# Kernel tuning notes

Hardware: AMD Instinct MI355X
Metric: run time of the kernel (lower is better)

The kernel has to match this reference:

```python
import jax, jax.numpy as jnp
import numpy as np

N = 32768      # nodes
E = 524288     # edges (avg degree 16)
F = 64         # node_feat_dim
D = 64         # gnn_dim (= per-head out channels, concat=False)
ED = 32        # edge_feat_dim
L = 6          # num_layers
H = 2          # heads
C = D          # per-head channels
LN_EPS = 1e-5


def layer_norm(h, g, b):
    mu = jnp.mean(h, axis=-1, keepdims=True)
    var = jnp.mean((h - mu) ** 2, axis=-1, keepdims=True)
    return g * (h - mu) * jax.lax.rsqrt(var + LN_EPS) + b


def setup_inputs() -> dict:
    key = jax.random.key(0)
    ks = jax.random.split(key, 16)
    x = jax.random.normal(ks[0], (N, F), jnp.float32)
    edge_index = jax.random.randint(ks[1], (2, E), 0, N, jnp.int32)
    edge_attr = jax.random.normal(ks[2], (E, ED), jnp.float32)
    manual_gamma = 1.0 + 0.1 * jax.random.normal(ks[3], (L, D), jnp.float32)
    manual_beta = 0.1 * jax.random.normal(ks[4], (L, D), jnp.float32)
    # node_embed Linear(F, D)
    embed_W = jax.random.normal(ks[5], (F, D), jnp.float32) / np.float32(np.sqrt(F))
    embed_b = jnp.zeros((D,), jnp.float32)
    # per-layer LayerNorm affine params
    ln_gamma = jnp.ones((L, D), jnp.float32)
    ln_beta = jnp.zeros((L, D), jnp.float32)
    # per-layer GATConv params (shared lin for src/dst, PyG non-bipartite)
    lin_W = jax.random.normal(ks[6], (L, D, H * C), jnp.float32) / np.float32(np.sqrt(D))
    lin_edge_W = jax.random.normal(ks[7], (L, ED, H * C), jnp.float32) / np.float32(np.sqrt(ED))
    att_src = jax.random.normal(ks[8], (L, H, C), jnp.float32) / np.float32(np.sqrt(C))
    att_dst = jax.random.normal(ks[9], (L, H, C), jnp.float32) / np.float32(np.sqrt(C))
    att_edge = jax.random.normal(ks[10], (L, H, C), jnp.float32) / np.float32(np.sqrt(C))
    gat_bias = jnp.zeros((L, C), jnp.float32)
    # edge output head: Linear(2D+ED, D) -> ReLU -> Linear(D, 1)
    head_W1 = jax.random.normal(ks[11], (2 * D + ED, D), jnp.float32) / np.float32(np.sqrt(2 * D + ED))
    head_b1 = jnp.zeros((D,), jnp.float32)
    head_W2 = jax.random.normal(ks[12], (D, 1), jnp.float32) / np.float32(np.sqrt(D))
    head_b2 = jnp.zeros((1,), jnp.float32)
    return dict(x=x, edge_index=edge_index, edge_attr=edge_attr,
                manual_gamma=manual_gamma, manual_beta=manual_beta,
                embed_W=embed_W, embed_b=embed_b, ln_gamma=ln_gamma, ln_beta=ln_beta,
                lin_W=lin_W, lin_edge_W=lin_edge_W, att_src=att_src, att_dst=att_dst,
                att_edge=att_edge, gat_bias=gat_bias, head_W1=head_W1, head_b1=head_b1,
                head_W2=head_W2, head_b2=head_b2)


def reference(x, edge_index, edge_attr, manual_gamma, manual_beta,
              embed_W, embed_b, ln_gamma, ln_beta, lin_W, lin_edge_W,
              att_src, att_dst, att_edge, gat_bias, head_W1, head_b1,
              head_W2, head_b2):
    src, dst = edge_index[0], edge_index[1]
    # PyG GATConv default add_self_loops=True, fill_value='mean' for edge_attr
    loop = jnp.arange(N, dtype=edge_index.dtype)
    src_f = jnp.concatenate([src, loop])   # [E+N]
    dst_f = jnp.concatenate([dst, loop])
    deg = jax.ops.segment_sum(jnp.ones((E,), x.dtype), dst, num_segments=N)
    loop_attr = jax.ops.segment_sum(edge_attr, dst, num_segments=N) / jnp.maximum(deg, 1.0)[:, None]
    edge_attr_f = jnp.concatenate([edge_attr, loop_attr], axis=0)  # [E+N, ED]

    h = x @ embed_W + embed_b  # [N, D]
    for l in range(L):
        hn = layer_norm(h, ln_gamma[l], ln_beta[l])
        hm = manual_gamma[l][None, :] * hn + manual_beta[l][None, :]
        xh = (hm @ lin_W[l]).reshape(N, H, C)                      # [N,H,C]
        a_s = jnp.sum(xh * att_src[l][None], axis=-1)              # [N,H]
        a_d = jnp.sum(xh * att_dst[l][None], axis=-1)              # [N,H]
        eh = (edge_attr_f @ lin_edge_W[l]).reshape(-1, H, C)       # [E+N,H,C]
        a_e = jnp.sum(eh * att_edge[l][None], axis=-1)             # [E+N,H]
        alpha = jax.nn.leaky_relu(a_s[src_f] + a_d[dst_f] + a_e, 0.2)
        amax = jax.ops.segment_max(alpha, dst_f, num_segments=N)   # every node has a self-loop
        ex = jnp.exp(alpha - amax[dst_f])
        den = jax.ops.segment_sum(ex, dst_f, num_segments=N)
        w = ex / (den[dst_f] + 1e-16)                              # segment softmax [E+N,H]
        msg = xh[src_f] * w[..., None]                             # [E+N,H,C]
        out = jax.ops.segment_sum(msg, dst_f, num_segments=N)      # [N,H,C]
        h = jax.nn.relu(jnp.mean(out, axis=1) + gat_bias[l])       # concat=False -> head mean

    ef = jnp.concatenate([h[src], h[dst], edge_attr], axis=-1)     # [E, 2D+ED]
    hid = jax.nn.relu(ef @ head_W1 + head_b1)
    return (hid @ head_W2 + head_b2)[:, 0]                         # [E]
```

## Files before the change

### kernel.cpp

```cpp
#include <hip/hip_runtime.h>
#include <hip/hip_bf16.h>
#include <math.h>

#define NN 32768
#define EE 524288
#define LL 6

typedef __attribute__((ext_vector_type(8))) short short8;
typedef __attribute__((ext_vector_type(4))) float floatx4;
typedef __attribute__((ext_vector_type(4))) float fx4;
typedef __attribute__((ext_vector_type(2))) float fx2;

union U16x8 { short8 v; unsigned short u[8]; };

__device__ __forceinline__ unsigned short f2bf(float x) {
    union { float f; unsigned int u; } v; v.f = x;
    unsigned int r = v.u + 0x7fffu + ((v.u >> 16) & 1u);
    return (unsigned short)(r >> 16);
}
__device__ __forceinline__ float bf2f(unsigned short h) {
    union { unsigned int u; float f; } v; v.u = (unsigned int)h << 16;
    return v.f;
}


__global__ void deg_kernel(const int* __restrict__ dst, int* __restrict__ deg) {
    int i = (blockIdx.x * 256 + threadIdx.x) * 4;
    int4 d = *(const int4*)(dst + i);
    atomicAdd(&deg[d.x], 1);
    atomicAdd(&deg[d.y], 1);
    atomicAdd(&deg[d.z], 1);
    atomicAdd(&deg[d.w], 1);
}

__global__ __launch_bounds__(1024) void scan_kernel(const int* __restrict__ deg,
                                                    int* __restrict__ row_ptr,
                                                    int* __restrict__ cnt) {
    __shared__ int bs[1024];
    int t = threadIdx.x;
    int base = t * 32;
    int loc[32];
    int s = 0;
#pragma unroll
    for (int i = 0; i < 32; ++i) { int v = deg[base + i]; loc[i] = s; s += v; }
    bs[t] = s;
    __syncthreads();
    for (int off = 1; off < 1024; off <<= 1) {
        int v = (t >= off) ? bs[t - off] : 0;
        __syncthreads();
        bs[t] += v;
        __syncthreads();
    }
    int pre = (t == 0) ? 0 : bs[t - 1];
#pragma unroll
    for (int i = 0; i < 32; ++i) { row_ptr[base + i] = pre + loc[i]; cnt[base + i] = 0; }
    if (t == 1023) row_ptr[NN] = bs[1023];
}

__global__ void fill_kernel(const int* __restrict__ src, const int* __restrict__ dst,
                            const int* __restrict__ row_ptr, int* __restrict__ cnt,
                            int2* __restrict__ sedge) {
    int e = blockIdx.x * 256 + threadIdx.x;
    if (e >= EE) return;
    int d = dst[e];
    int pos = row_ptr[d] + atomicAdd(&cnt[d], 1);
    sedge[pos] = make_int2(e, src[e]);
}

__global__ __launch_bounds__(256) void smallprep_kernel(
    const float* __restrict__ lin_W, const float* __restrict__ head_W1,
    const float* __restrict__ lin_edge_W, const float* __restrict__ att_edge,
    const float* __restrict__ att_src, const float* __restrict__ att_dst,
    unsigned short* __restrict__ gBhi, unsigned short* __restrict__ gBlo,
    unsigned short* __restrict__ aeBhi, unsigned short* __restrict__ aeBlo,
    float* __restrict__ vs, float* __restrict__ vvd,
    unsigned short* __restrict__ w1chi, unsigned short* __restrict__ w1clo,
    int* __restrict__ deg) {
    __shared__ float svb[384];
    int bb = blockIdx.x;
    int tid = threadIdx.x;
    if (bb < 7) {
        unsigned short* dh = gBhi + (size_t)bb * 128 * 64;
        unsigned short* dl = gBlo + (size_t)bb * 128 * 64;
        if (bb < 6) {
            int n2 = tid & 63, kh = tid >> 6;
            U16x8 hh[4], ll[4];
            for (int kk = 0; kk < 32; ++kk) {
                int j = kh * 32 + kk;
                int h = j >> 6, k = j & 63;
                float wv = 0.5f * lin_W[((size_t)bb * 64 + k) * 128 + h * 64 + n2];
                unsigned short h16 = f2bf(wv);
                hh[kk >> 3].u[kk & 7] = h16;
                ll[kk >> 3].u[kk & 7] = f2bf(wv - bf2f(h16));
            }
#pragma unroll
            for (int c = 0; c < 4; ++c) {
                int cg = kh * 4 + c;
                int off = n2 * 128 + ((cg ^ (n2 & 15)) << 3);
                *(short8*)(dh + off) = hh[c].v;
                *(short8*)(dl + off) = ll[c].v;
            }
        } else {
            int n = tid & 127, kh = tid >> 7;
            U16x8 hh[4], ll[4];
            for (int kk = 0; kk < 32; ++kk) {
                int k = kh * 32 + kk;
                float wv = (n < 64) ? head_W1[k * 64 + n] : head_W1[(64 + k) * 64 + (n - 64)];
                unsigned short h16 = f2bf(wv);
                hh[kk >> 3].u[kk & 7] = h16;
                ll[kk >> 3].u[kk & 7] = f2bf(wv - bf2f(h16));
            }
#pragma unroll
            for (int c = 0; c < 4; ++c) {
                int cg = kh * 4 + c;
                int off = n * 64 + ((cg ^ (n & 7)) << 3);
                *(short8*)(dh + off) = hh[c].v;
                *(short8*)(dl + off) = ll[c].v;
            }
        }
    } else if (bb == 7) {
        for (int t = tid; t < 384; t += 256) {
            int l = t / 64; int r = t & 63; int ed = r >> 1; int hh = r & 1;
            const float* w = lin_edge_W + l * 32 * 128 + ed * 128 + hh * 64;
            const float* a = att_edge + l * 128 + hh * 64;
            float s = 0.f;
#pragma unroll 8
            for (int c = 0; c < 64; ++c) s += w[c] * a[c];
            svb[t] = s;
        }
        int n = tid & 63, kc = tid >> 6;
#pragma unroll
        for (int j = 0; j < 8; ++j) {
            int k = kc * 8 + j;
            float wv = head_W1[(128 + k) * 64 + n];
            unsigned short h16 = f2bf(wv);
            w1chi[n * 32 + k] = h16;
            w1clo[n * 32 + k] = f2bf(wv - bf2f(h16));
        }
        __syncthreads();
        if (tid < 64) {
            int n2 = tid & 15, q = tid >> 4;
            U16x8 hi, lo;
#pragma unroll
            for (int i = 0; i < 8; ++i) {
                int k = q * 8 + i;
                float val = (n2 < 12) ? svb[(n2 >> 1) * 64 + k * 2 + (n2 & 1)] : 0.f;
                unsigned short h16 = f2bf(val);
                hi.u[i] = h16;
                lo.u[i] = f2bf(val - bf2f(h16));
            }
            *(short8*)(aeBhi + tid * 8) = hi.v;
            *(short8*)(aeBlo + tid * 8) = lo.v;
        }
    } else if (bb < 14) {
        int l = bb - 8;
        int sel = tid >> 7, idx = tid & 127;
        int h = idx >> 6, k = idx & 63;
        const float* att = (sel ? att_dst : att_src) + l * 128 + h * 64;
        const float* wr = lin_W + ((size_t)l * 64 + k) * 128 + h * 64;
        float s = 0.f;
#pragma unroll 8
        for (int c = 0; c < 64; ++c) s += wr[c] * att[c];
        (sel ? vvd : vs)[l * 128 + idx] = s;
    } else {
        int i = (bb - 14) * 1024 + tid * 4;
        *(int4*)(deg + i) = make_int4(0, 0, 0, 0);
    }
}

__global__ __launch_bounds__(256) void ae_csr_kernel(
    const float* __restrict__ edge_attr, const int2* __restrict__ sedge,
    const unsigned short* __restrict__ aeBhi, const unsigned short* __restrict__ aeBlo,
    float* __restrict__ aeF, int* __restrict__ srcc) {
    __shared__ float tr[4][64 * 13];
    int tid = threadIdx.x;
    int w = tid >> 6, lane = tid & 63;
    int p0 = blockIdx.x * 256 + w * 64;
    short8 bhi = *(const short8*)(aeBhi + lane * 8);
    short8 blo = *(const short8*)(aeBlo + lane * 8);
    int r = lane & 15, q = lane >> 4;
    float* trw = tr[w];
#pragma unroll
    for (int t = 0; t < 4; ++t) {
        int eg = sedge[p0 + t * 16 + r].x;
        const fx4* p = (const fx4*)(edge_attr + (size_t)eg * 32 + q * 8);
        fx4 f0 = p[0], f1 = p[1];
        float av[8] = {f0.x, f0.y, f0.z, f0.w, f1.x, f1.y, f1.z, f1.w};
        U16x8 hi, lo;
#pragma unroll
        for (int jj = 0; jj < 8; ++jj) {
            unsigned short h16 = f2bf(av[jj]);
            hi.u[jj] = h16;
            lo.u[jj] = f2bf(av[jj] - bf2f(h16));
        }
        floatx4 acc = {};
        acc = __builtin_amdgcn_mfma_f32_16x16x32_bf16(lo.v, bhi, acc, 0, 0, 0);
        acc = __builtin_amdgcn_mfma_f32_16x16x32_bf16(hi.v, blo, acc, 0, 0, 0);
        acc = __builtin_amdgcn_mfma_f32_16x16x32_bf16(hi.v, bhi, acc, 0, 0, 0);
        if (r < 12) {
#pragma unroll
            for (int rr = 0; rr < 4; ++rr)
                trw[(t * 16 + q * 4 + rr) * 13 + r] = acc[rr];
        }
    }
    int2 sl = sedge[p0 + lane];
    srcc[p0 + lane] = sl.y;
#pragma unroll
    for (int l = 0; l < LL; ++l) {
        fx2 rec;
        rec.x = trw[lane * 13 + l * 2];
        rec.y = trw[lane * 13 + l * 2 + 1];
        __builtin_nontemporal_store(rec, (fx2*)(aeF + ((size_t)l * EE + p0 + lane) * 2));
    }
}

__global__ __launch_bounds__(256) void embed_ln_kernel(
    const float* __restrict__ x, const float* __restrict__ W, const float* __restrict__ b,
    const float* __restrict__ ln_g, const float* __restrict__ ln_b,
    const float* __restrict__ mg, const float* __restrict__ mb,
    const float* __restrict__ vs0, const float* __restrict__ vd0,
    unsigned short* __restrict__ hm_bf, float* __restrict__ a_s, float* __restrict__ a_d) {
    __shared__ float xr[4][64];
    int w = threadIdx.x >> 6, j = threadIdx.x & 63;
    int n = blockIdx.x * 4 + w;
    xr[w][j] = x[(size_t)n * 64 + j];
    __syncthreads();
    float acc = b[j];
#pragma unroll 8
    for (int k = 0; k < 64; ++k) acc += xr[w][k] * W[k * 64 + j];
    float s = acc, sq = acc * acc;
    for (int off = 1; off < 64; off <<= 1) { s += __shfl_xor(s, off); sq += __shfl_xor(sq, off); }
    float mu = s * (1.f / 64.f);
    float var = sq * (1.f / 64.f) - mu * mu;
    float rs = rsqrtf(var + 1e-5f);
    float hm = mg[j] * (ln_g[j] * (acc - mu) * rs + ln_b[j]) + mb[j];
    hm_bf[(size_t)n * 64 + j] = f2bf(hm);
    float s0 = hm * vs0[j], s1 = hm * vs0[64 + j];
    float d0 = hm * vd0[j], d1 = hm * vd0[64 + j];
    for (int off = 1; off < 64; off <<= 1) {
        s0 += __shfl_xor(s0, off); s1 += __shfl_xor(s1, off);
        d0 += __shfl_xor(d0, off); d1 += __shfl_xor(d1, off);
    }
    if (j == 0) {
        a_s[n * 2] = s0; a_s[n * 2 + 1] = s1;
        a_d[n * 2] = d0; a_d[n * 2 + 1] = d1;
    }
}

__device__ __forceinline__ void fma8h(uint4 pv, float w, float* a) {
    unsigned int u[4] = {pv.x, pv.y, pv.z, pv.w};
#pragma unroll
    for (int q = 0; q < 4; ++q) {
        union { unsigned int x; float f; } lo, hi;
        lo.x = u[q] << 16; hi.x = u[q] & 0xffff0000u;
        a[2 * q]     += w * lo.f;
        a[2 * q + 1] += w * hi.f;
    }
}

__device__ __forceinline__ void agg_node2(
    int n, int ch, const uint4* hmv, const float2* as2,
    const float* ad_in, const float* aeLl, const int* srcc,
    const int* row_ptr, float* sg, U16x8& hb0, U16x8& hb1) {
    float2 adn = ((const float2*)ad_in)[n];
    float2 asn = as2[n];
    uint4 pvself = hmv[(size_t)n * 8 + ch];
    int beg = row_ptr[n], end = row_ptr[n + 1];
    int degn = end - beg;
    float acc0[8] = {}, acc1[8] = {};
    float den0 = 0.f, den1 = 0.f, aex = 0.f, aey = 0.f;
    for (int base = 0; base < degn; base += 16) {
        int cnt = degn - base; cnt = cnt > 16 ? 16 : cnt;
#pragma unroll
        for (int pass = 0; pass < 2; ++pass) {
            int s = pass * 8 + ch;
            float w0v = 0.f, w1v = 0.f;
            int sval = 0;
            if (s < cnt) {
                int idx = beg + base + s;
                int sv = srcc[idx];
                fx2 ae = *(const fx2*)(aeLl + (size_t)idx * 2);
                float2 as = as2[sv];
                aex += ae.x; aey += ae.y;
                float al0 = as.x + adn.x + ae.x; al0 = al0 > 0.f ? al0 : 0.2f * al0;
                float al1 = as.y + adn.y + ae.y; al1 = al1 > 0.f ? al1 : 0.2f * al1;
                w0v = __expf(al0);
                w1v = __expf(al1);
                sval = sv;
            }
            float4 st;
            st.x = __int_as_float(sval); st.y = w0v; st.z = w1v; st.w = 0.f;
            *(float4*)(sg + s * 4) = st;
        }
        int c8 = (cnt + 7) & ~7;
        for (int s = 0; s < c8; s += 8) {
            float4 m[8];
#pragma unroll
            for (int u = 0; u < 8; ++u) m[u] = *(const float4*)(sg + (s + u) * 4);
            uint4 p[8];
#pragma unroll
            for (int u = 0; u < 8; ++u) p[u] = hmv[(size_t)__float_as_int(m[u].x) * 8 + ch];
#pragma unroll
            for (int u = 0; u < 8; ++u) {
                den0 += m[u].y; fma8h(p[u], m[u].y, acc0);
                den1 += m[u].z; fma8h(p[u], m[u].z, acc1);
            }
        }
    }
#pragma unroll
    for (int m2 = 1; m2 < 8; m2 <<= 1) {
        aex += __shfl_xor(aex, m2);
        aey += __shfl_xor(aey, m2);
    }
    float invd = 1.f / fmaxf((float)degn, 1.f);
    float al0 = asn.x + adn.x + aex * invd; al0 = al0 > 0.f ? al0 : 0.2f * al0;
    float al1 = asn.y + adn.y + aey * invd; al1 = al1 > 0.f ? al1 : 0.2f * al1;
    float ws0 = __expf(al0), ws1 = __expf(al1);
    den0 += ws0; den1 += ws1;
    fma8h(pvself, ws0, acc0);
    fma8h(pvself, ws1, acc1);
    float inv0 = 1.f / (den0 + 1e-16f), inv1 = 1.f / (den1 + 1e-16f);
#pragma unroll
    for (int q = 0; q < 8; ++q) {
        hb0.u[q] = f2bf(acc0[q] * inv0);
        hb1.u[q] = f2bf(acc1[q] * inv1);
    }
}

__global__ __launch_bounds__(512) void fused_post(
    const unsigned short* __restrict__ hm_in, const float* __restrict__ as_in,
    const float* __restrict__ ad_in, const float* __restrict__ aeLl,
    const int* __restrict__ srcc, const int* __restrict__ row_ptr,
    const unsigned short* __restrict__ gBhi, const unsigned short* __restrict__ gBlo,
    const float* __restrict__ bias, const float* __restrict__ ln_g,
    const float* __restrict__ ln_b, const float* __restrict__ mg,
    const float* __restrict__ mb, const float* __restrict__ vsn,
    const float* __restrict__ vdn, unsigned short* __restrict__ hm_out,
    float* __restrict__ as_out, float* __restrict__ ad_out) {
    __shared__ char smem[49152];
    unsigned short* Ahi = (unsigned short*)smem;
    float* stgAll = (float*)(smem + 16384);
    unsigned short* Bhi = (unsigned short*)(smem + 16384);
    unsigned short* Blo = (unsigned short*)(smem + 32768);
    int tid = threadIdx.x;
    int w = tid >> 6, lane = tid & 63;
    int g = lane >> 3, ch = lane & 7;
    const float2* as2 = (const float2*)as_in;
    const uint4* hmv = (const uint4*)hm_in;
    float* sg = stgAll + (w * 8 + g) * 64;
    int nb = blockIdx.x * 64;

    {
        int m = w * 8 + g;
        U16x8 hb0, hb1;
        agg_node2(nb + m, ch, hmv, as2, ad_in, aeLl, srcc, row_ptr, sg, hb0, hb1);
        *(short8*)(Ahi + m * 128 + ((ch ^ (m & 15)) << 3)) = hb0.v;
        *(short8*)(Ahi + m * 128 + (((8 + ch) ^ (m & 15)) << 3)) = hb1.v;
    }
    __syncthreads();
    {
        const uint4* sh = (const uint4*)gBhi;
        const uint4* sl = (const uint4*)gBlo;
        for (int i = tid; i < 1024; i += 512) {
            ((uint4*)Bhi)[i] = sh[i];
            ((uint4*)Blo)[i] = sl[i];
        }
    }
    __syncthreads();

    if (w < 4) {
        int col = lane & 15, quad = lane >> 4;
        int m = w * 16 + col;
        floatx4 acc[4] = {};
#pragma unroll
        for (int s = 0; s < 4; ++s) {
            int ca = (quad + 4 * s) ^ col;
            short8 ahi = *(const short8*)(Ahi + m * 128 + ca * 8);
#pragma unroll
            for (int t = 0; t < 4; ++t) {
                int off = (t * 16 + col) * 128 + ca * 8;
                short8 bhi = *(const short8*)(Bhi + off);
                short8 blo = *(const short8*)(Blo + off);
                acc[t] = __builtin_amdgcn_mfma_f32_16x16x32_bf16(ahi, blo, acc[t], 0, 0, 0);
                acc[t] = __builtin_amdgcn_mfma_f32_16x16x32_bf16(ahi, bhi, acc[t], 0, 0, 0);
            }
        }
        int nodebase = nb + w * 16;
        float bv[4];
#pragma unroll
        for (int t = 0; t < 4; ++t) bv[t] = bias[t * 16 + col];
        float vsv[4], vsv1[4], vdv[4], vdv1[4], lg[4], lb[4], mgv[4], mbv[4];
#pragma unroll
        for (int t = 0; t < 4; ++t) {
            int c = t * 16 + col;
            vsv[t] = vsn[c]; vsv1[t] = vsn[64 + c];
            vdv[t] = vdn[c]; vdv1[t] = vdn[64 + c];
            lg[t] = ln_g[c]; lb[t] = ln_b[c];
            mgv[t] = mg[c]; mbv[t] = mb[c];
        }
#pragma unroll
        for (int r = 0; r < 4; ++r) {
            int node = nodebase + quad * 4 + r;
            float hv[4];
            float s = 0.f, sq = 0.f;
#pragma unroll
            for (int t = 0; t < 4; ++t) {
                float v = acc[t][r] + bv[t];
                v = v > 0.f ? v : 0.f;
                hv[t] = v;
                s += v; sq += v * v;
            }
            for (int off = 1; off < 16; off <<= 1) { s += __shfl_xor(s, off); sq += __shfl_xor(sq, off); }
            float mu = s * (1.f / 64.f);
            float var = sq * (1.f / 64.f) - mu * mu;
            float rs = rsqrtf(var + 1e-5f);
            float s0 = 0.f, s1 = 0.f, d0 = 0.f, d1 = 0.f;
#pragma unroll
            for (int t = 0; t < 4; ++t) {
                float hmval = mgv[t] * (lg[t] * (hv[t] - mu) * rs + lb[t]) + mbv[t];
                hm_out[(size_t)node * 64 + t * 16 + col] = f2bf(hmval);
                s0 += hmval * vsv[t]; s1 += hmval * vsv1[t];
                d0 += hmval * vdv[t]; d1 += hmval * vdv1[t];
            }
            for (int off = 1; off < 16; off <<= 1) {
                s0 += __shfl_xor(s0, off); s1 += __shfl_xor(s1, off);
                d0 += __shfl_xor(d0, off); d1 += __shfl_xor(d1, off);
            }
            if (col == 0) {
                as_out[node * 2] = s0; as_out[node * 2 + 1] = s1;
                ad_out[node * 2] = d0; ad_out[node * 2 + 1] = d1;
            }
        }
    }
}

__global__ __launch_bounds__(512) void fused_uv(
    const unsigned short* __restrict__ hm_in, const float* __restrict__ as_in,
    const float* __restrict__ ad_in, const float* __restrict__ aeLl,
    const int* __restrict__ srcc, const int* __restrict__ row_ptr,
    const unsigned short* __restrict__ gB5hi, const unsigned short* __restrict__ gB5lo,
    const float* __restrict__ bias,
    const unsigned short* __restrict__ gB6hi, const unsigned short* __restrict__ gB6lo,
    unsigned short* __restrict__ uv) {
    __shared__ char smem[49152];
    unsigned short* Ahi  = (unsigned short*)smem;
    float* stgAll        = (float*)(smem + 16384);
    unsigned short* B5hi = (unsigned short*)(smem + 16384);
    unsigned short* B5lo = (unsigned short*)(smem + 32768);
    unsigned short* A2hi = (unsigned short*)smem;
    unsigned short* A2lo = (unsigned short*)(smem + 8192);
    unsigned short* B6hi = (unsigned short*)(smem + 16384);
    unsigned short* B6lo = (unsigned short*)(smem + 32768);
    int tid = threadIdx.x;
    int w = tid >> 6, lane = tid & 63;
    int g = lane >> 3, ch = lane & 7;
    const float2* as2 = (const float2*)as_in;
    const uint4* hmv = (const uint4*)hm_in;
    float* sg = stgAll + (w * 8 + g) * 64;
    int nb = blockIdx.x * 64;

    {
        int m = w * 8 + g;
        U16x8 hb0, hb1;
        agg_node2(nb + m, ch, hmv, as2, ad_in, aeLl, srcc, row_ptr, sg, hb0, hb1);
        *(short8*)(Ahi + m * 128 + ((ch ^ (m & 15)) << 3)) = hb0.v;
        *(short8*)(Ahi + m * 128 + (((8 + ch) ^ (m & 15)) << 3)) = hb1.v;
    }
    __syncthreads();
    {
        const uint4* sh = (const uint4*)gB5hi;
        const uint4* sl = (const uint4*)gB5lo;
        for (int i = tid; i < 1024; i += 512) {
            ((uint4*)B5hi)[i] = sh[i];
            ((uint4*)B5lo)[i] = sl[i];
        }
    }
    __syncthreads();

    int col = lane & 15, quad = lane >> 4;
    int m = w * 16 + col;
    floatx4 acc[4] = {};
    if (w < 4) {
#pragma unroll
        for (int s = 0; s < 4; ++s) {
            int ca = (quad + 4 * s) ^ col;
            short8 ahi = *(const short8*)(Ahi + m * 128 + ca * 8);
#pragma unroll
            for (int t = 0; t < 4; ++t) {
                int off = (t * 16 + col) * 128 + ca * 8;
                short8 bhi = *(const short8*)(B5hi + off);
                short8 blo = *(const short8*)(B5lo + off);
                acc[t] = __builtin_amdgcn_mfma_f32_16x16x32_bf16(ahi, blo, acc[t], 0, 0, 0);
                acc[t] = __builtin_amdgcn_mfma_f32_16x16x32_bf16(ahi, bhi, acc[t], 0, 0, 0);
            }
        }
    }
    __syncthreads();
    if (w < 4) {
        float bv[4];
#pragma unroll
        for (int t = 0; t < 4; ++t) bv[t] = bias[t * 16 + col];
#pragma unroll
        for (int t = 0; t < 4; ++t) {
            int c = t * 16 + col;
            int cg = c >> 3, cr = c & 7;
#pragma unroll
            for (int r = 0; r < 4; ++r) {
                float v = acc[t][r] + bv[t];
                v = v > 0.f ? v : 0.f;
                int i = w * 16 + quad * 4 + r;
                int off = i * 64 + ((cg ^ (i & 7)) << 3) + cr;
                unsigned short hhv = f2bf(v);
                A2hi[off] = hhv;
                A2lo[off] = f2bf(v - bf2f(hhv));
            }
        }
    }
    for (int i = tid; i < 1024; i += 512) {
        ((uint4*)B6hi)[i] = ((const uint4*)gB6hi)[i];
        ((uint4*)B6lo)[i] = ((const uint4*)gB6lo)[i];
    }
    __syncthreads();

    if (w < 4) {
        floatx4 acc2[8] = {};
#pragma unroll
        for (int s = 0; s < 2; ++s) {
            int ca = (quad + 4 * s) ^ (col & 7);
            short8 a2h = *(const short8*)(A2hi + m * 64 + ca * 8);
            short8 a2l = *(const short8*)(A2lo + m * 64 + ca * 8);
#pragma unroll
            for (int t = 0; t < 8; ++t) {
                int off = (t * 16 + col) * 64 + ca * 8;
                short8 bh = *(const short8*)(B6hi + off);
                short8 bl = *(const short8*)(B6lo + off);
                acc2[t] = __builtin_amdgcn_mfma_f32_16x16x32_bf16(a2l, bh, acc2[t], 0, 0, 0);
                acc2[t] = __builtin_amdgcn_mfma_f32_16x16x32_bf16(a2h, bl, acc2[t], 0, 0, 0);
                acc2[t] = __builtin_amdgcn_mfma_f32_16x16x32_bf16(a2h, bh, acc2[t], 0, 0, 0);
            }
        }
        int nodebase = nb + w * 16;
#pragma unroll
        for (int t = 0; t < 8; ++t)
#pragma unroll
            for (int r = 0; r < 4; ++r)
                uv[(size_t)(nodebase + quad * 4 + r) * 128 + t * 16 + col] = f2bf(acc2[t][r]);
    }
}

__global__ __launch_bounds__(256) void head2_kernel(
    const unsigned short* __restrict__ uv, const int* __restrict__ src,
    const int* __restrict__ dst, const float* __restrict__ edge_attr,
    const unsigned short* __restrict__ w1chi, const unsigned short* __restrict__ w1clo,
    const float* __restrict__ b1, const float* __restrict__ W2,
    const float* __restrict__ b2, float* __restrict__ out) {
    __shared__ float g[64][68];
    __shared__ unsigned short Abf[64 * 40];
    __shared__ unsigned short Bh[64 * 40], Bl[64 * 40];
    __shared__ int sA[64], dA[64];
    int tid = threadIdx.x;
    int base = blockIdx.x * 64;
    if (tid < 64) sA[tid] = src[base + tid];
    else if (tid < 128) dA[tid - 64] = dst[base + tid - 64];
    {
        int n = tid >> 2, c = tid & 3;
        *(short8*)(Bh + n * 40 + c * 8) = *(const short8*)(w1chi + n * 32 + c * 8);
        *(short8*)(Bl + n * 40 + c * 8) = *(const short8*)(w1clo + n * 32 + c * 8);
    }
    {
        int e = tid >> 2, q = tid & 3;
        const fx4* p = (const fx4*)(edge_attr + (size_t)(base + e) * 32 + q * 8);
        fx4 f0 = __builtin_nontemporal_load(p);
        fx4 f1 = __builtin_nontemporal_load(p + 1);
        float av[8] = {f0.x, f0.y, f0.z, f0.w, f1.x, f1.y, f1.z, f1.w};
        U16x8 cv;
#pragma unroll
        for (int jj = 0; jj < 8; ++jj) cv.u[jj] = f2bf(av[jj]);
        *(short8*)(Abf + e * 40 + q * 8) = cv.v;
    }
    __syncthreads();
    {
        int e = tid >> 2, q = tid & 3;
        const uint4* su = (const uint4*)(uv + (size_t)sA[e] * 128);
        const uint4* dv = (const uint4*)(uv + (size_t)dA[e] * 128);
        uint4 U0 = su[2 * q], U1 = su[2 * q + 1];
        uint4 V0 = dv[8 + 2 * q], V1 = dv[9 + 2 * q];
        const float4* b1p = (const float4*)(b1 + q * 16);
        float bb[16];
#pragma unroll
        for (int jj = 0; jj < 4; ++jj) {
            float4 b4 = b1p[jj];
            bb[4 * jj] = b4.x; bb[4 * jj + 1] = b4.y; bb[4 * jj + 2] = b4.z; bb[4 * jj + 3] = b4.w;
        }
        unsigned int uw[8] = {U0.x, U0.y, U0.z, U0.w, U1.x, U1.y, U1.z, U1.w};
        unsigned int vw[8] = {V0.x, V0.y, V0.z, V0.w, V1.x, V1.y, V1.z, V1.w};
        float* gr = &g[e][q * 16];
#pragma unroll
        for (int jj = 0; jj < 8; ++jj) {
            gr[2 * jj] = bf2f((unsigned short)(uw[jj] & 0xffff)) +
                         bf2f((unsigned short)(vw[jj] & 0xffff)) + bb[2 * jj];
            gr[2 * jj + 1] = bf2f((unsigned short)(uw[jj] >> 16)) +
                             bf2f((unsigned short)(vw[jj] >> 16)) + bb[2 * jj + 1];
        }
    }
    __syncthreads();

    int lane = tid & 63, w = tid >> 6, col = lane & 15, quad = lane >> 4;
    short8 a = *(const short8*)(Abf + (w * 16 + col) * 40 + quad * 8);
    floatx4 acc[4] = {};
#pragma unroll
    for (int t = 0; t < 4; ++t) {
        int off = (t * 16 + col) * 40 + quad * 8;
        short8 bh = *(const short8*)(Bh + off);
        short8 bl = *(const short8*)(Bl + off);
        acc[t] = __builtin_amdgcn_mfma_f32_16x16x32_bf16(a, bl, acc[t], 0, 0, 0);
        acc[t] = __builtin_amdgcn_mfma_f32_16x16x32_bf16(a, bh, acc[t], 0, 0, 0);
    }
    float sv[4] = {0.f, 0.f, 0.f, 0.f};
#pragma unroll
    for (int t = 0; t < 4; ++t) {
        float w2v = W2[t * 16 + col];
#pragma unroll
        for (int r = 0; r < 4; ++r) {
            float hid = acc[t][r] + g[w * 16 + quad * 4 + r][t * 16 + col];
            hid = hid > 0.f ? hid : 0.f;
            sv[r] += hid * w2v;
        }
    }
    float b2v = b2[0];
#pragma unroll
    for (int r = 0; r < 4; ++r) {
        float v = sv[r];
        v += __shfl_xor(v, 1);
        v += __shfl_xor(v, 2);
        v += __shfl_xor(v, 4);
        v += __shfl_xor(v, 8);
        if (col == 0) out[base + w * 16 + quad * 4 + r] = v + b2v;
    }
}


extern "C" void kernel_launch(void* const* d_in, const int* in_sizes, int n_in,
                              void* d_out, int out_size, void* d_ws, size_t ws_size,
                              hipStream_t stream) {
    const float* x            = (const float*)d_in[0];
    const int*   edge_index   = (const int*)d_in[1];
    const float* edge_attr    = (const float*)d_in[2];
    const float* manual_gamma = (const float*)d_in[3];
    const float* manual_beta  = (const float*)d_in[4];
    const float* embed_W      = (const float*)d_in[5];
    const float* embed_b      = (const float*)d_in[6];
    const float* ln_gamma     = (const float*)d_in[7];
    const float* ln_beta      = (const float*)d_in[8];
    const float* lin_W        = (const float*)d_in[9];
    const float* lin_edge_W   = (const float*)d_in[10];
    const float* att_src      = (const float*)d_in[11];
    const float* att_dst      = (const float*)d_in[12];
    const float* att_edge     = (const float*)d_in[13];
    const float* gat_bias     = (const float*)d_in[14];
    const float* head_W1      = (const float*)d_in[15];
    const float* head_b1      = (const float*)d_in[16];
    const float* head_W2      = (const float*)d_in[17];
    const float* head_b2      = (const float*)d_in[18];
    float* out = (float*)d_out;

    const int* src = edge_index;
    const int* dst = edge_index + EE;

    char* ws = (char*)d_ws;
    size_t off = 0;
    auto alloc = [&](size_t bytes) {
        void* p = ws + off;
        off += (bytes + 255) & ~(size_t)255;
        return p;
    };
    int*   deg        = (int*)alloc(NN * 4);
    int*   row_ptr    = (int*)alloc((NN + 1) * 4);
    int*   cnt        = (int*)alloc(NN * 4);
    int2*  sedge      = (int2*)alloc((size_t)EE * 8);
    int*   srcc       = (int*)alloc((size_t)EE * 4);
    float* aeF        = (float*)alloc((size_t)LL * EE * 8);
    float* vs         = (float*)alloc(LL * 128 * 4);
    float* vvd        = (float*)alloc(LL * 128 * 4);
    float* asA        = (float*)alloc((size_t)NN * 2 * 4);
    float* asB        = (float*)alloc((size_t)NN * 2 * 4);
    float* adA        = (float*)alloc((size_t)NN * 2 * 4);
    float* adB        = (float*)alloc((size_t)NN * 2 * 4);
    unsigned short* hmA   = (unsigned short*)alloc((size_t)NN * 64 * 2);
    unsigned short* hmB   = (unsigned short*)alloc((size_t)NN * 64 * 2);
    unsigned short* uvbuf = (unsigned short*)alloc((size_t)NN * 128 * 2);
    unsigned short* gBhi  = (unsigned short*)alloc((size_t)7 * 128 * 64 * 2);
    unsigned short* gBlo  = (unsigned short*)alloc((size_t)7 * 128 * 64 * 2);
    unsigned short* w1chi = (unsigned short*)alloc(64 * 32 * 2);
    unsigned short* w1clo = (unsigned short*)alloc(64 * 32 * 2);
    unsigned short* aeBhi = (unsigned short*)alloc(64 * 8 * 2);
    unsigned short* aeBlo = (unsigned short*)alloc(64 * 8 * 2);
    if (off > ws_size) return;

    smallprep_kernel<<<46, 256, 0, stream>>>(lin_W, head_W1, lin_edge_W, att_edge,
                                             att_src, att_dst, gBhi, gBlo, aeBhi, aeBlo,
                                             vs, vvd, w1chi, w1clo, deg);
    deg_kernel<<<EE / 1024, 256, 0, stream>>>(dst, deg);
    scan_kernel<<<1, 1024, 0, stream>>>(deg, row_ptr, cnt);
    fill_kernel<<<EE / 256, 256, 0, stream>>>(src, dst, row_ptr, cnt, sedge);
    ae_csr_kernel<<<EE / 256, 256, 0, stream>>>(edge_attr, sedge, aeBhi, aeBlo, aeF, srcc);
    embed_ln_kernel<<<NN / 4, 256, 0, stream>>>(x, embed_W, embed_b, ln_gamma, ln_beta,
                                                manual_gamma, manual_beta, vs, vvd,
                                                hmA, asA, adA);

    for (int l = 0; l < LL; ++l) {
        const unsigned short* hin = (l & 1) ? hmB : hmA;
        unsigned short* hout = (l & 1) ? hmA : hmB;
        const float* asi = (l & 1) ? asB : asA;
        float* aso = (l & 1) ? asA : asB;
        const float* adi = (l & 1) ? adB : adA;
        float* ado = (l & 1) ? adA : adB;
        const float* aeLl = aeF + (size_t)l * EE * 2;
        if (l < LL - 1) {
            fused_post<<<NN / 64, 512, 0, stream>>>(
                hin, asi, adi, aeLl, srcc, row_ptr,
                gBhi + (size_t)l * 128 * 64, gBlo + (size_t)l * 128 * 64,
                gat_bias + l * 64, ln_gamma + (l + 1) * 64, ln_beta + (l + 1) * 64,
                manual_gamma + (l + 1) * 64, manual_beta + (l + 1) * 64,
                vs + (l + 1) * 128, vvd + (l + 1) * 128, hout, aso, ado);
        } else {
            fused_uv<<<NN / 64, 512, 0, stream>>>(
                hin, asi, adi, aeLl, srcc, row_ptr,
                gBhi + (size_t)l * 128 * 64, gBlo + (size_t)l * 128 * 64,
                gat_bias + l * 64, gBhi + (size_t)6 * 128 * 64,
                gBlo + (size_t)6 * 128 * 64, uvbuf);
        }
    }

    head2_kernel<<<EE / 64, 256, 0, stream>>>(uvbuf, src, dst, edge_attr, w1chi, w1clo,
                                              head_b1, head_W2, head_b2, out);
}
```

Measured before the change: 424.7 us.

## Relabel nodes by in-degree bins to balance GAT aggregation work

Replaces the single-block CSR prefix scan with a degree histogram, a bin scan and a rank kernel. Together these renumber every node so that nodes with equal in-degree sit next to each other, and the CSR row pointers follow directly from the bin offsets. Node features, attention scalars, source indices and the edge head all use the new rank. The layer kernels process blocks in reverse order, so the highest-degree nodes are scheduled first. The goal is to reduce load imbalance and divergence in the per-node aggregation loops. The cost is extra small kernels, extra atomics and one more index indirection. Degrees are clamped to 127, which would corrupt the CSR if any node had more in-edges than that.

```diff
diff --git a/kernel.cpp b/kernel.cpp
--- a/kernel.cpp
+++ b/kernel.cpp
@@ -33,38 +33,48 @@
     atomicAdd(&deg[d.w], 1);
 }
 
-__global__ __launch_bounds__(1024) void scan_kernel(const int* __restrict__ deg,
-                                                    int* __restrict__ row_ptr,
-                                                    int* __restrict__ cnt) {
-    __shared__ int bs[1024];
-    int t = threadIdx.x;
-    int base = t * 32;
-    int loc[32];
-    int s = 0;
-#pragma unroll
-    for (int i = 0; i < 32; ++i) { int v = deg[base + i]; loc[i] = s; s += v; }
-    bs[t] = s;
-    __syncthreads();
-    for (int off = 1; off < 1024; off <<= 1) {
-        int v = (t >= off) ? bs[t - off] : 0;
-        __syncthreads();
-        bs[t] += v;
-        __syncthreads();
-    }
-    int pre = (t == 0) ? 0 : bs[t - 1];
-#pragma unroll
-    for (int i = 0; i < 32; ++i) { row_ptr[base + i] = pre + loc[i]; cnt[base + i] = 0; }
-    if (t == 1023) row_ptr[NN] = bs[1023];
+__global__ void hist_kernel(const int* __restrict__ deg, int* __restrict__ hist) {
+    int n = blockIdx.x * 256 + threadIdx.x;
+    int b = deg[n]; b = b > 127 ? 127 : b;
+    atomicAdd(&hist[b], 1);
+}
+
+__global__ __launch_bounds__(128) void binscan_kernel(const int* __restrict__ hist,
+                                                      int* __restrict__ binBase,
+                                                      int* __restrict__ edgeBase) {
+    if (threadIdx.x == 0) {
+        int accN = 0, accE = 0;
+        for (int b = 0; b < 128; ++b) {
+            binBase[b] = accN;
+            edgeBase[b] = accE;
+            int c = hist[b];
+            accN += c;
+            accE += c * b;
+        }
+    }
+}
+
+__global__ void rank_kernel(const int* __restrict__ deg, const int* __restrict__ binBase,
+                            const int* __restrict__ edgeBase, int* __restrict__ binCnt,
+                            int* __restrict__ rank, int* __restrict__ row_ptrP,
+                            int* __restrict__ cnt) {
+    int n = blockIdx.x * 256 + threadIdx.x;
+    int b = deg[n]; b = b > 127 ? 127 : b;
+    int r = binBase[b] + atomicAdd(&binCnt[b], 1);
+    rank[n] = r;
+    row_ptrP[r] = edgeBase[b] + (r - binBase[b]) * b;
+    cnt[r] = 0;
+    if (n == 0) row_ptrP[NN] = EE;
 }
 
 __global__ void fill_kernel(const int* __restrict__ src, const int* __restrict__ dst,
-                            const int* __restrict__ row_ptr, int* __restrict__ cnt,
-                            int2* __restrict__ sedge) {
+                            const int* __restrict__ rank, const int* __restrict__ row_ptrP,
+                            int* __restrict__ cnt, int2* __restrict__ sedge) {
     int e = blockIdx.x * 256 + threadIdx.x;
     if (e >= EE) return;
-    int d = dst[e];
-    int pos = row_ptr[d] + atomicAdd(&cnt[d], 1);
-    sedge[pos] = make_int2(e, src[e]);
+    int rd = rank[dst[e]];
+    int pos = row_ptrP[rd] + atomicAdd(&cnt[rd], 1);
+    sedge[pos] = make_int2(e, rank[src[e]]);
 }
 
 __global__ __launch_bounds__(256) void smallprep_kernel(
@@ -75,7 +85,7 @@
     unsigned short* __restrict__ aeBhi, unsigned short* __restrict__ aeBlo,
     float* __restrict__ vs, float* __restrict__ vvd,
     unsigned short* __restrict__ w1chi, unsigned short* __restrict__ w1clo,
-    int* __restrict__ deg) {
+    int* __restrict__ deg, int* __restrict__ hist, int* __restrict__ binCnt) {
     __shared__ float svb[384];
     int bb = blockIdx.x;
     int tid = threadIdx.x;
@@ -162,9 +172,11 @@
 #pragma unroll 8
         for (int c = 0; c < 64; ++c) s += wr[c] * att[c];
         (sel ? vvd : vs)[l * 128 + idx] = s;
-    } else {
+    } else if (bb < 46) {
         int i = (bb - 14) * 1024 + tid * 4;
         *(int4*)(deg + i) = make_int4(0, 0, 0, 0);
+    } else {
+        if (tid < 128) { hist[tid] = 0; binCnt[tid] = 0; }
     }
 }
 
@@ -219,6 +231,7 @@
     const float* __restrict__ ln_g, const float* __restrict__ ln_b,
     const float* __restrict__ mg, const float* __restrict__ mb,
     const float* __restrict__ vs0, const float* __restrict__ vd0,
+    const int* __restrict__ rank,
     unsigned short* __restrict__ hm_bf, float* __restrict__ a_s, float* __restrict__ a_d) {
     __shared__ float xr[4][64];
     int w = threadIdx.x >> 6, j = threadIdx.x & 63;
@@ -234,7 +247,8 @@
     float var = sq * (1.f / 64.f) - mu * mu;
     float rs = rsqrtf(var + 1e-5f);
     float hm = mg[j] * (ln_g[j] * (acc - mu) * rs + ln_b[j]) + mb[j];
-    hm_bf[(size_t)n * 64 + j] = f2bf(hm);
+    int rp = rank[n];
+    hm_bf[(size_t)rp * 64 + j] = f2bf(hm);
     float s0 = hm * vs0[j], s1 = hm * vs0[64 + j];
     float d0 = hm * vd0[j], d1 = hm * vd0[64 + j];
     for (int off = 1; off < 64; off <<= 1) {
@@ -242,8 +256,8 @@
         d0 += __shfl_xor(d0, off); d1 += __shfl_xor(d1, off);
     }
     if (j == 0) {
-        a_s[n * 2] = s0; a_s[n * 2 + 1] = s1;
-        a_d[n * 2] = d0; a_d[n * 2 + 1] = d1;
+        a_s[rp * 2] = s0; a_s[rp * 2 + 1] = s1;
+        a_d[rp * 2] = d0; a_d[rp * 2 + 1] = d1;
     }
 }
 
@@ -348,7 +362,7 @@
     const float2* as2 = (const float2*)as_in;
     const uint4* hmv = (const uint4*)hm_in;
     float* sg = stgAll + (w * 8 + g) * 64;
-    int nb = blockIdx.x * 64;
+    int nb = NN - 64 - blockIdx.x * 64;
 
     {
         int m = w * 8 + g;
@@ -457,7 +471,7 @@
     const float2* as2 = (const float2*)as_in;
     const uint4* hmv = (const uint4*)hm_in;
     float* sg = stgAll + (w * 8 + g) * 64;
-    int nb = blockIdx.x * 64;
+    int nb = NN - 64 - blockIdx.x * 64;
 
     {
         int m = w * 8 + g;
@@ -550,7 +564,8 @@
 
 __global__ __launch_bounds__(256) void head2_kernel(
     const unsigned short* __restrict__ uv, const int* __restrict__ src,
-    const int* __restrict__ dst, const float* __restrict__ edge_attr,
+    const int* __restrict__ dst, const int* __restrict__ rank,
+    const float* __restrict__ edge_attr,
     const unsigned short* __restrict__ w1chi, const unsigned short* __restrict__ w1clo,
     const float* __restrict__ b1, const float* __restrict__ W2,
     const float* __restrict__ b2, float* __restrict__ out) {
@@ -560,8 +575,8 @@
     __shared__ int sA[64], dA[64];
     int tid = threadIdx.x;
     int base = blockIdx.x * 64;
-    if (tid < 64) sA[tid] = src[base + tid];
-    else if (tid < 128) dA[tid - 64] = dst[base + tid - 64];
+    if (tid < 64) sA[tid] = rank[src[base + tid]];
+    else if (tid < 128) dA[tid - 64] = rank[dst[base + tid - 64]];
     {
         int n = tid >> 2, c = tid & 3;
         *(short8*)(Bh + n * 40 + c * 8) = *(const short8*)(w1chi + n * 32 + c * 8);
@@ -675,6 +690,11 @@
         return p;
     };
     int*   deg        = (int*)alloc(NN * 4);
+    int*   hist       = (int*)alloc(128 * 4);
+    int*   binBase    = (int*)alloc(128 * 4);
+    int*   edgeBase   = (int*)alloc(128 * 4);
+    int*   binCnt     = (int*)alloc(128 * 4);
+    int*   rankA      = (int*)alloc(NN * 4);
     int*   row_ptr    = (int*)alloc((NN + 1) * 4);
     int*   cnt        = (int*)alloc(NN * 4);
     int2*  sedge      = (int2*)alloc((size_t)EE * 8);
@@ -697,16 +717,19 @@
     unsigned short* aeBlo = (unsigned short*)alloc(64 * 8 * 2);
     if (off > ws_size) return;
 
-    smallprep_kernel<<<46, 256, 0, stream>>>(lin_W, head_W1, lin_edge_W, att_edge,
+    smallprep_kernel<<<47, 256, 0, stream>>>(lin_W, head_W1, lin_edge_W, att_edge,
                                              att_src, att_dst, gBhi, gBlo, aeBhi, aeBlo,
-                                             vs, vvd, w1chi, w1clo, deg);
+                                             vs, vvd, w1chi, w1clo, deg, hist, binCnt);
     deg_kernel<<<EE / 1024, 256, 0, stream>>>(dst, deg);
-    scan_kernel<<<1, 1024, 0, stream>>>(deg, row_ptr, cnt);
-    fill_kernel<<<EE / 256, 256, 0, stream>>>(src, dst, row_ptr, cnt, sedge);
+    hist_kernel<<<NN / 256, 256, 0, stream>>>(deg, hist);
+    binscan_kernel<<<1, 128, 0, stream>>>(hist, binBase, edgeBase);
+    rank_kernel<<<NN / 256, 256, 0, stream>>>(deg, binBase, edgeBase, binCnt,
+                                              rankA, row_ptr, cnt);
+    fill_kernel<<<EE / 256, 256, 0, stream>>>(src, dst, rankA, row_ptr, cnt, sedge);
     ae_csr_kernel<<<EE / 256, 256, 0, stream>>>(edge_attr, sedge, aeBhi, aeBlo, aeF, srcc);
     embed_ln_kernel<<<NN / 4, 256, 0, stream>>>(x, embed_W, embed_b, ln_gamma, ln_beta,
                                                 manual_gamma, manual_beta, vs, vvd,
-                                                hmA, asA, adA);
+                                                rankA, hmA, asA, adA);
 
     for (int l = 0; l < LL; ++l) {
         const unsigned short* hin = (l & 1) ? hmB : hmA;
@@ -732,6 +755,7 @@
         }
     }
 
-    head2_kernel<<<EE / 64, 256, 0, stream>>>(uvbuf, src, dst, edge_attr, w1chi, w1clo,
-                                              head_b1, head_W2, head_b2, out);
-}
+    head2_kernel<<<EE / 64, 256, 0, stream>>>(uvbuf, src, dst, rankA, edge_attr,
+                                              w1chi, w1clo, head_b1, head_W2,
+                                              head_b2, out);
+}
```

After: 588.9 us. +38.7%, slower.
